# Kernel optimization log

Measured on AMD Instinct MI355X. Metric: run time of the kernel, lower is better.

The kernel has to match this reference:

```python
import jax, jax.numpy as jnp
import numpy as np
import math

D = 768
H = 12
HD = D // H  # 64


def setup_inputs() -> dict:
    key = jax.random.key(0)
    ks = jax.random.split(key, 8)
    B, S = 32, 127
    desc = jax.random.normal(ks[0], (B, S, D), dtype=jnp.float32)
    nv = jax.random.normal(ks[1], (B, S + 1, D), dtype=jnp.float32)
    def xavier(k, shape):
        fan_in, fan_out = shape[1], shape[0]
        gain = 1.0 / math.sqrt(2.0)
        limit = gain * math.sqrt(6.0 / (fan_in + fan_out))
        return jax.random.uniform(k, shape, jnp.float32, -limit, limit)
    Wq = xavier(ks[2], (D, D)); bq = jnp.zeros((D,), jnp.float32)
    Wk = xavier(ks[3], (D, D)); bk = jnp.zeros((D,), jnp.float32)
    Wv = xavier(ks[4], (D, D)); bv = jnp.zeros((D,), jnp.float32)
    # attn_proj: Linear(3*head_dim, 1)
    Wa = xavier(ks[5], (1, 3 * HD))[0]  # [3*HD]
    ba = jnp.zeros((), jnp.float32)
    return {
        "desc_embeddings": desc,
        "name_value_embeddings": nv,
        "Wq": Wq, "bq": bq, "Wk": Wk, "bk": bk, "Wv": Wv, "bv": bv,
        "Wa": Wa, "ba": ba,
    }


def _forward(desc_embeddings, name_value_embeddings, Wq, bq, Wk, bk, Wv, bv, Wa, ba):
    B, new_seq, _ = name_value_embeddings.shape
    S = new_seq - 1

    # adjacency: var-var all ones, CLS->Var row = 1, Var->CLS col = 0, CLS->CLS = 0
    adj = jnp.zeros((new_seq, new_seq), jnp.float32)
    adj = adj.at[1:, 1:].set(1.0)
    adj = adj.at[0, 1:].set(1.0)
    adj = jnp.broadcast_to(adj, (B, new_seq, new_seq))

    # q,k,v: [B, H, new_seq, HD]
    def proj(W, b):
        y = name_value_embeddings @ W.T + b
        return y.reshape(B, new_seq, H, HD).transpose(0, 2, 1, 3)
    q = proj(Wq, bq); k = proj(Wk, bk); v = proj(Wv, bv)

    # attn_proj weight split: [q_part | k_part | edge_part], each [HD]
    wq_a, wk_a, we_a = Wa[:HD], Wa[HD:2 * HD], Wa[2 * HD:]

    # q/k scalar contributions per (b,h,i) and (b,h,j)
    lq = jnp.einsum('bhid,d->bhi', q, wq_a)  # [B,H,new_seq]
    lk = jnp.einsum('bhjd,d->bhj', k, wk_a)  # [B,H,new_seq]

    # edge_attr[b,i,j] per head h (head slice of concat[node_i_desc, node_j_desc]):
    # edge vector = concat(desc_i, desc_j)[h*HD:(h+1)*HD] viewed as [H, HD] of 2D dims.
    # concat(desc_i, desc_j) has 2D dims -> reshaped to [H, HD] means head h takes
    # slice [h*HD:(h+1)*HD] of the 2D-dim concat. Heads 0..H/2-1 come from desc_i,
    # heads H/2..H-1 come from desc_j. Compute edge dot with we_a accordingly.
    # desc_full[b,t] : [B,S,D]. Build per-head contributions:
    # for h < H//2: edge slice = desc_i[h*HD:(h+1)*HD]  -> depends only on i
    # for h >= H//2: edge slice = desc_j[(h-H//2)*HD:(h-H//2+1)*HD] -> depends only on j
    desc_heads = desc_embeddings.reshape(B, S, H // 2, 2 * HD)  # wrong split; do directly
    # Direct: per head h, slice indices into the 2D concat vector
    dh = desc_embeddings.reshape(B, S, H, HD)  # desc split into H chunks of HD (covers D = H*HD)
    # concat(desc_i,desc_j) reshaped to [H,HD]: heads 0..H/2-1 use dh_i[:, :, h],
    # heads H/2..H-1 use dh_j[:, :, h - H/2]
    e_dot = jnp.einsum('bshd,d->bsh', dh, jnp.broadcast_to(we_a, (HD,)))  # placeholder, recompute per head below
    # per-head edge scalar contribution for var-var edges:
    ei = jnp.einsum('bshd,d->bhs', dh, we_a)  # contribution if head slice comes from desc at position s
    Hh = H // 2
    # var-var logits edge part: for h<Hh depends on i; for h>=Hh depends on j
    le_i = ei[:, :Hh, :]   # [B,Hh,S] depends on i (row)
    le_j = ei[:, Hh:, :]   # [B,Hh,S] depends on j (col)

    # CLS edges: cls_edge_attr = concat(desc, desc) at position t (the var index)
    # row 0 (CLS->var j): edge = concat(desc_j, desc_j) -> head h slice:
    #   h<Hh: dh_j[h]; h>=Hh: dh_j[h-Hh]  -> scalar ei[b,h,j] with h mapped
    e_cls = jnp.concatenate([ei[:, :Hh, :], ei[:, :Hh, :]], axis=1) * 0  # init
    e_cls = jnp.concatenate([le_i, le_i], axis=1)  # [B,H,S]: head h<Hh uses dh[h], h>=Hh uses dh[h-Hh]
    # note ei[:, :Hh] corresponds to dh chunks 0..Hh-1 ; for h>=Hh slice is dh[h-Hh] -> same le_i

    # Assemble full logits [B,H,new_seq,new_seq]
    logits = lq[:, :, :, None] + lk[:, :, None, :]
    # edge contributions (only where adj==1; edge_attr zeroed elsewhere by mask mult)
    edge = jnp.zeros((B, H, new_seq, new_seq), jnp.float32)
    # var-var block [1:,1:]
    ev = jnp.zeros((B, H, S, S), jnp.float32)
    ev = ev + jnp.pad(le_i, ((0, 0), (0, Hh), (0, 0)))[:, :, :, None] * 0  # keep shapes
    ev_i = jnp.concatenate([le_i, jnp.zeros_like(le_j)], axis=1)  # h<Hh: i-dependent
    ev_j = jnp.concatenate([jnp.zeros_like(le_i), le_j], axis=1)  # h>=Hh: j-dependent
    ev = ev_i[:, :, :, None] + ev_j[:, :, None, :]  # [B,H,S,S]
    edge = edge.at[:, :, 1:, 1:].set(ev)
    # CLS row (0, 1:): cls_edge = concat(desc_j,desc_j); j = column var
    edge = edge.at[:, :, 0, 1:].set(e_cls)
    # CLS col (1:, 0): cls_edge = concat(desc_i,desc_i) BUT adj[:,1:,0]=0 so edge_attr
    # multiplied by adj -> zero; also masked out. edge stays 0, but torch zeroes it too.
    # mask edge by adjacency (edge_attr *= adj)
    edge = edge * adj[:, None, :, :]
    logits = logits + edge + ba

    mask = (adj[:, None, :, :] == 0).astype(jnp.float32) * -1e9
    logits = logits + mask
    attn = jax.nn.softmax(logits, axis=-1)  # [B,H,new_seq,new_seq]
    ctx = jnp.einsum('bhij,bhjd->bhid', attn, v)
    basis_outputs = ctx.transpose(0, 2, 1, 3)  # [B,new_seq,H,HD]
    return basis_outputs, attn


def reference(desc_embeddings, name_value_embeddings, Wq, bq, Wk, bk, Wv, bv, Wa, ba):
    return _forward(desc_embeddings, name_value_embeddings, Wq, bq, Wk, bk, Wv, bv, Wa, ba)
```

## Files before the change

kernel.cpp:

```cpp
#include <hip/hip_runtime.h>

#define NB 32
#define NS 128
#define SD 127
#define ND 768
#define NH 12
#define HD 64

__device__ inline float wredSum(float v){
  #pragma unroll
  for (int off=32; off>0; off>>=1) v += __shfl_xor(v, off);
  return v;
}
__device__ inline float wredMax(float v){
  #pragma unroll
  for (int off=32; off>0; off>>=1) v = fmaxf(v, __shfl_xor(v, off));
  return v;
}

__global__ __launch_bounds__(256)
void fold_ei(const float* __restrict__ Wk, const float* __restrict__ bk,
             const float* __restrict__ desc, const float* __restrict__ Wa,
             float* __restrict__ uk, float* __restrict__ bkdot,
             float* __restrict__ ei){
  int blk = blockIdx.x, t = threadIdx.x;
  int wave = t >> 6, lane = t & 63;
  if (blk < 144){
    __shared__ float red[4][64];
    int h = blk/12, cb = blk%12;
    int c0 = t & 63, dg = t >> 6;
    const float* base = Wk + (size_t)(h*HD + dg*16)*ND + cb*64 + c0;
    float acc = 0.f;
    #pragma unroll
    for (int i=0;i<16;++i) acc += base[(size_t)i*ND] * Wa[64 + dg*16 + i];
    red[dg][c0] = acc;
    __syncthreads();
    if (dg==0) uk[h*ND + cb*64 + c0] = red[0][c0]+red[1][c0]+red[2][c0]+red[3][c0];
    if (blk==0 && t < NH){
      float a = 0.f;
      for (int d=0; d<64; ++d) a += bk[t*HD+d]*Wa[64+d];
      bkdot[t] = a;
    }
  } else {
    int bs = blk - 144;
    int b = bs / SD, s = bs % SD;
    float wea = Wa[128 + lane];
    const float* row = desc + (size_t)bs * ND;
    #pragma unroll
    for (int hh=0; hh<3; ++hh){
      int h = wave + hh*4;
      float v = row[h*HD + lane] * wea;
      v = wredSum(v);
      if (lane==0) ei[(size_t)(b*NH + h)*NS + s] = v;
    }
  }
}

__global__ __launch_bounds__(256)
void lk_kernel(const float* __restrict__ nv, const float* __restrict__ uk,
               const float* __restrict__ bkdot, float* __restrict__ lk){
  __shared__ __align__(16) float S[4*ND];
  int blk = blockIdx.x, t = threadIdx.x, wave = t>>6, lane = t&63;
  float ukr[3][12], bkd[3];
  #pragma unroll
  for (int hh=0; hh<3; ++hh){
    int h = wave*3 + hh;
    bkd[hh] = bkdot[h];
    #pragma unroll
    for (int k=0;k<12;++k) ukr[hh][k] = uk[h*ND + lane + 64*k];
  }
  int j0 = blk*4;
  const float4* src = (const float4*)(nv + (size_t)j0*ND);
  ((float4*)S)[t]     = src[t];
  ((float4*)S)[t+256] = src[t+256];
  ((float4*)S)[t+512] = src[t+512];
  __syncthreads();
  float acc[12];
  #pragma unroll
  for (int rr=0; rr<4; ++rr){
    #pragma unroll
    for (int hh=0; hh<3; ++hh){
      float a = 0.f;
      #pragma unroll
      for (int k=0;k<12;++k) a += S[rr*ND + lane + 64*k]*ukr[hh][k];
      acc[rr*3+hh] = a;
    }
  }
  #pragma unroll
  for (int i=0;i<12;++i) acc[i] = wredSum(acc[i]);
  if (lane == 0){
    int b = j0 >> 7, jb = j0 & 127;
    #pragma unroll
    for (int rr=0; rr<4; ++rr)
      #pragma unroll
      for (int hh=0; hh<3; ++hh)
        lk[(size_t)(b*NH + wave*3 + hh)*NS + jb + rr] = acc[rr*3+hh] + bkd[hh];
  }
}

__global__ __launch_bounds__(256)
void msoft_attn(const float* __restrict__ nv, const float* __restrict__ lk,
                const float* __restrict__ ei, float* __restrict__ m_part,
                float* __restrict__ out){
  int blk = blockIdx.x;
  int b = blk >> 3, jg = blk & 7;
  int t = threadIdx.x, wave = t >> 6, lane = t & 63;
  __shared__ float slk[NH*NS];
  __shared__ float sei[NH*NS];
  __shared__ float wf[24][NS];
  for (int i=t; i<NH*NS; i+=256) slk[i] = lk[(size_t)b*NH*NS + i];
  for (int i=t; i<NH*NS; i+=256) sei[i] = ei[(size_t)b*NH*NS + i];
  __syncthreads();
  #pragma unroll
  for (int rr=0; rr<6; ++rr){
    int r = wave*6 + rr;
    int h = r >> 1, which = r & 1;
    const float* eirow = (which==0) ? (sei + (h%6)*NS) : (sei + h*NS);
    float g = (which==0) ? 1.f : (h>=6 ? 1.f : 0.f);
    float x0 = (lane>=1) ? slk[h*NS+lane] + g*eirow[lane-1] : -3.0e38f;
    float x1 = slk[h*NS+lane+64] + g*eirow[lane+63];
    float mm = wredMax(fmaxf(x0,x1));
    float e0 = (lane>=1) ? __expf(x0-mm) : 0.f;
    float e1 = __expf(x1-mm);
    float s  = wredSum(e0+e1);
    float inv = 1.f/s;
    wf[r][lane]    = e0*inv;
    wf[r][lane+64] = e1*inv;
  }
  __syncthreads();
  if (t < 192){
    const float4* nvb = (const float4*)(nv + ((size_t)b*NS + jg*16)*ND);
    float4 acc[24];
    #pragma unroll
    for (int r=0;r<24;++r) acc[r] = make_float4(0.f,0.f,0.f,0.f);
    #pragma unroll 2
    for (int jj=0; jj<16; ++jj){
      float4 x = nvb[jj*192 + t];
      int j = jg*16 + jj;
      #pragma unroll
      for (int r=0;r<24;++r){
        float wr = wf[r][j];
        acc[r].x += wr*x.x; acc[r].y += wr*x.y;
        acc[r].z += wr*x.z; acc[r].w += wr*x.w;
      }
    }
    #pragma unroll
    for (int r=0;r<24;++r)
      ((float4*)(m_part + ((size_t)(b*24 + r)*8 + jg)*ND))[t] = acc[r];
  }
  float* abase = out + (size_t)NB*NS*ND + (size_t)(b*NH)*NS*NS;
  for (int idx=t; idx<6144; idx+=256){
    int h = idx >> 9;
    int rem = idx & 511;
    int il = rem >> 5, q = rem & 31;
    int i = jg*16 + il;
    const float* srcw = (i==0) ? wf[h*2] : wf[h*2+1];
    float4 v = { srcw[q*4], srcw[q*4+1], srcw[q*4+2], srcw[q*4+3] };
    ((float4*)(abase + (size_t)h*NS*NS))[i*32 + q] = v;
  }
}

__global__ __launch_bounds__(256)
void proj_basis(const float* __restrict__ m_part, const float* __restrict__ Wv,
                const float* __restrict__ bv, float* __restrict__ out){
  int bh = blockIdx.x;
  int b = bh / NH, h = bh % NH;
  int t = threadIdx.x, wave = t >> 6, lane = t & 63;
  __shared__ float msum0[ND], msum1[ND];
  __shared__ float cvec[2*HD];
  for (int i=t; i<2*ND; i+=256){
    int rl = (i >= ND);
    int c  = i - rl*ND;
    const float* mp = m_part + ((size_t)(b*24 + h*2 + rl)*8)*ND + c;
    float s = 0.f;
    #pragma unroll
    for (int g8=0; g8<8; ++g8) s += mp[(size_t)g8*ND];
    (rl ? msum1 : msum0)[c] = s;
  }
  __syncthreads();
  #pragma unroll
  for (int dd=0; dd<16; ++dd){
    int d = wave*16 + dd;
    const float* wvr = Wv + (size_t)(h*HD + d)*ND;
    float p0=0.f, p1=0.f;
    #pragma unroll
    for (int k=0; k<12; ++k){
      float wv = wvr[lane + 64*k];
      p0 += wv*msum0[lane + 64*k];
      p1 += wv*msum1[lane + 64*k];
    }
    p0 = wredSum(p0); p1 = wredSum(p1);
    if (lane==0){
      float bb = bv[h*HD + d];
      cvec[d]    = p0 + bb;
      cvec[64+d] = p1 + bb;
    }
  }
  __syncthreads();
  float* bo = out + (size_t)b*NS*ND + h*HD;
  #pragma unroll
  for (int k=0;k<8;++k){
    int idx = t + k*256;
    int i = idx>>4, q = idx&15;
    const float* srcc = (i==0) ? cvec : cvec+64;
    float4 v = { srcc[q*4], srcc[q*4+1], srcc[q*4+2], srcc[q*4+3] };
    *(float4*)(bo + (size_t)i*ND + q*4) = v;
  }
}

extern "C" void kernel_launch(void* const* d_in, const int* in_sizes, int n_in,
                              void* d_out, int out_size, void* d_ws, size_t ws_size,
                              hipStream_t stream) {
  const float* desc = (const float*)d_in[0];
  const float* nv   = (const float*)d_in[1];
  const float* Wk   = (const float*)d_in[4];
  const float* bk   = (const float*)d_in[5];
  const float* Wv   = (const float*)d_in[6];
  const float* bv   = (const float*)d_in[7];
  const float* Wa   = (const float*)d_in[8];
  float* out = (float*)d_out;
  float* ws  = (float*)d_ws;

  float* uk     = ws;
  float* bkdot  = ws + 9216;
  float* eibuf  = ws + 9232;
  float* lkbuf  = ws + 58384;
  float* m_part = ws + 107536;

  fold_ei   <<<4208, 256, 0, stream>>>(Wk, bk, desc, Wa, uk, bkdot, eibuf);
  lk_kernel <<<1024, 256, 0, stream>>>(nv, uk, bkdot, lkbuf);
  msoft_attn<<<256,  256, 0, stream>>>(nv, lkbuf, eibuf, m_part, out);
  proj_basis<<<384,  256, 0, stream>>>(m_part, Wv, bv, out);
}
```

Baseline: 138.7 us.

## Fuse Wv projection into attention kernel with atomic accumulation and last-block output

Removes the separate proj_basis kernel and the m_part global buffer. Each attention block now owns a 96-column slice of the feature dimension: it reduces its weighted sums in shared memory, multiplies them by the matching Wv slice, and atomically adds the partial results into a per-batch ctx buffer that the first kernel pre-fills with bv. A per-batch counter lets the last finishing block broadcast ctx into the basis output. This saves a kernel launch and the m_part round trip through global memory, at the cost of float atomics, non-deterministic summation order, and extra barriers.

```diff
diff --git a/kernel.cpp b/kernel.cpp
--- a/kernel.cpp
+++ b/kernel.cpp
@@ -19,10 +19,12 @@
 }
 
 __global__ __launch_bounds__(256)
-void fold_ei(const float* __restrict__ Wk, const float* __restrict__ bk,
-             const float* __restrict__ desc, const float* __restrict__ Wa,
-             float* __restrict__ uk, float* __restrict__ bkdot,
-             float* __restrict__ ei){
+void fold_ei_init(const float* __restrict__ Wk, const float* __restrict__ bk,
+                  const float* __restrict__ desc, const float* __restrict__ Wa,
+                  const float* __restrict__ bv,
+                  float* __restrict__ uk, float* __restrict__ bkdot,
+                  float* __restrict__ ei, float* __restrict__ ctx,
+                  int* __restrict__ cnt){
   int blk = blockIdx.x, t = threadIdx.x;
   int wave = t >> 6, lane = t & 63;
   if (blk < 144){
@@ -41,7 +43,7 @@
       for (int d=0; d<64; ++d) a += bk[t*HD+d]*Wa[64+d];
       bkdot[t] = a;
     }
-  } else {
+  } else if (blk < 144 + NB*SD){
     int bs = blk - 144;
     int b = bs / SD, s = bs % SD;
     float wea = Wa[128 + lane];
@@ -53,6 +55,15 @@
       v = wredSum(v);
       if (lane==0) ei[(size_t)(b*NH + h)*NS + s] = v;
     }
+  } else {
+    int idx = (blk - (144 + NB*SD))*256 + t;
+    int rem = idx % 384;
+    int r = rem >> 4, q = rem & 15;
+    int h = r >> 1;
+    const float* bb = bv + h*HD + q*4;
+    float4 v = { bb[0], bb[1], bb[2], bb[3] };
+    ((float4*)ctx)[idx] = v;
+    if (blk == 144 + NB*SD && t < NB) cnt[t] = 0;
   }
 }
 
@@ -77,7 +88,7 @@
   __syncthreads();
   float acc[12];
   #pragma unroll
-  for (int rr=0; rr<4; ++rr){
+  for (int rr=0; rr<4; ++rr)
     #pragma unroll
     for (int hh=0; hh<3; ++hh){
       float a = 0.f;
@@ -85,7 +96,6 @@
       for (int k=0;k<12;++k) a += S[rr*ND + lane + 64*k]*ukr[hh][k];
       acc[rr*3+hh] = a;
     }
-  }
   #pragma unroll
   for (int i=0;i<12;++i) acc[i] = wredSum(acc[i]);
   if (lane == 0){
@@ -99,15 +109,22 @@
 }
 
 __global__ __launch_bounds__(256)
-void msoft_attn(const float* __restrict__ nv, const float* __restrict__ lk,
-                const float* __restrict__ ei, float* __restrict__ m_part,
-                float* __restrict__ out){
+void fused(const float* __restrict__ nv, const float* __restrict__ lk,
+           const float* __restrict__ ei, const float* __restrict__ Wv,
+           float* __restrict__ ctx, int* __restrict__ cnt,
+           float* __restrict__ out){
   int blk = blockIdx.x;
-  int b = blk >> 3, jg = blk & 7;
+  int b = blk >> 3, cc = blk & 7;
   int t = threadIdx.x, wave = t >> 6, lane = t & 63;
-  __shared__ float slk[NH*NS];
-  __shared__ float sei[NH*NS];
-  __shared__ float wf[24][NS];
+  __shared__ __align__(16) float S[13104];
+  __shared__ int flag;
+  float* slk  = S;
+  float* sei  = S + 1536;
+  float* wf   = S + 3072;
+  float* mred = S + 6144;
+  float* m    = S + 10752;
+  float* ctxb = S + 6144;
+
   for (int i=t; i<NH*NS; i+=256) slk[i] = lk[(size_t)b*NH*NS + i];
   for (int i=t; i<NH*NS; i+=256) sei[i] = ei[(size_t)b*NH*NS + i];
   __syncthreads();
@@ -124,87 +141,108 @@
     float e1 = __expf(x1-mm);
     float s  = wredSum(e0+e1);
     float inv = 1.f/s;
-    wf[r][lane]    = e0*inv;
-    wf[r][lane+64] = e1*inv;
-  }
+    wf[r*NS + lane]    = e0*inv;
+    wf[r*NS + lane+64] = e1*inv;
+  }
+
+  float4 acc[24];
+  #pragma unroll
+  for (int r=0;r<24;++r) acc[r] = make_float4(0.f,0.f,0.f,0.f);
+  int col = t % 24, jg = t / 24;
   __syncthreads();
   if (t < 192){
-    const float4* nvb = (const float4*)(nv + ((size_t)b*NS + jg*16)*ND);
-    float4 acc[24];
-    #pragma unroll
-    for (int r=0;r<24;++r) acc[r] = make_float4(0.f,0.f,0.f,0.f);
+    const float4* nvb = (const float4*)nv;
     #pragma unroll 2
     for (int jj=0; jj<16; ++jj){
-      float4 x = nvb[jj*192 + t];
       int j = jg*16 + jj;
+      float4 x = nvb[(size_t)(b*NS + j)*192 + cc*24 + col];
       #pragma unroll
       for (int r=0;r<24;++r){
-        float wr = wf[r][j];
+        float wr = wf[r*NS + j];
         acc[r].x += wr*x.x; acc[r].y += wr*x.y;
         acc[r].z += wr*x.z; acc[r].w += wr*x.w;
       }
     }
-    #pragma unroll
-    for (int r=0;r<24;++r)
-      ((float4*)(m_part + ((size_t)(b*24 + r)*8 + jg)*ND))[t] = acc[r];
-  }
+  }
+  #pragma unroll
+  for (int p=0; p<4; ++p){
+    __syncthreads();
+    if (t < 192){
+      #pragma unroll
+      for (int rr=0; rr<6; ++rr)
+        ((float4*)mred)[(rr*24 + col)*8 + jg] = acc[p*6+rr];
+    }
+    __syncthreads();
+    if (t < 144){
+      int rr = t / 24, c2 = t % 24;
+      float4 s = make_float4(0.f,0.f,0.f,0.f);
+      #pragma unroll
+      for (int g=0; g<8; ++g){
+        float4 v = ((float4*)mred)[(rr*24 + c2)*8 + g];
+        s.x += v.x; s.y += v.y; s.z += v.z; s.w += v.w;
+      }
+      int r = p*6 + rr;
+      m[r*97 + c2*4+0] = s.x; m[r*97 + c2*4+1] = s.y;
+      m[r*97 + c2*4+2] = s.z; m[r*97 + c2*4+3] = s.w;
+    }
+  }
+  __syncthreads();
+
+  #pragma unroll
+  for (int i=0; i<3; ++i){
+    int hd = t*3 + i;
+    int h = hd >> 6, d = hd & 63;
+    const float4* wr = (const float4*)(Wv + (size_t)hd*ND + cc*96);
+    const float* m0 = m + (2*h)*97;
+    const float* m1 = m0 + 97;
+    float p0=0.f, p1=0.f;
+    #pragma unroll
+    for (int c4=0; c4<24; ++c4){
+      float4 wv4 = wr[c4];
+      int c = c4*4;
+      p0 += wv4.x*m0[c] + wv4.y*m0[c+1] + wv4.z*m0[c+2] + wv4.w*m0[c+3];
+      p1 += wv4.x*m1[c] + wv4.y*m1[c+1] + wv4.z*m1[c+2] + wv4.w*m1[c+3];
+    }
+    atomicAdd(&ctx[(size_t)(b*24 + 2*h    )*HD + d], p0);
+    atomicAdd(&ctx[(size_t)(b*24 + 2*h + 1)*HD + d], p1);
+  }
+
   float* abase = out + (size_t)NB*NS*ND + (size_t)(b*NH)*NS*NS;
   for (int idx=t; idx<6144; idx+=256){
     int h = idx >> 9;
     int rem = idx & 511;
     int il = rem >> 5, q = rem & 31;
-    int i = jg*16 + il;
-    const float* srcw = (i==0) ? wf[h*2] : wf[h*2+1];
+    int i = cc*16 + il;
+    const float* srcw = (i==0) ? (wf + h*2*NS) : (wf + (h*2+1)*NS);
     float4 v = { srcw[q*4], srcw[q*4+1], srcw[q*4+2], srcw[q*4+3] };
     ((float4*)(abase + (size_t)h*NS*NS))[i*32 + q] = v;
   }
-}
-
-__global__ __launch_bounds__(256)
-void proj_basis(const float* __restrict__ m_part, const float* __restrict__ Wv,
-                const float* __restrict__ bv, float* __restrict__ out){
-  int bh = blockIdx.x;
-  int b = bh / NH, h = bh % NH;
-  int t = threadIdx.x, wave = t >> 6, lane = t & 63;
-  __shared__ float msum0[ND], msum1[ND];
-  __shared__ float cvec[2*HD];
-  for (int i=t; i<2*ND; i+=256){
-    int rl = (i >= ND);
-    int c  = i - rl*ND;
-    const float* mp = m_part + ((size_t)(b*24 + h*2 + rl)*8)*ND + c;
-    float s = 0.f;
-    #pragma unroll
-    for (int g8=0; g8<8; ++g8) s += mp[(size_t)g8*ND];
-    (rl ? msum1 : msum0)[c] = s;
-  }
-  __syncthreads();
-  #pragma unroll
-  for (int dd=0; dd<16; ++dd){
-    int d = wave*16 + dd;
-    const float* wvr = Wv + (size_t)(h*HD + d)*ND;
-    float p0=0.f, p1=0.f;
-    #pragma unroll
-    for (int k=0; k<12; ++k){
-      float wv = wvr[lane + 64*k];
-      p0 += wv*msum0[lane + 64*k];
-      p1 += wv*msum1[lane + 64*k];
-    }
-    p0 = wredSum(p0); p1 = wredSum(p1);
-    if (lane==0){
-      float bb = bv[h*HD + d];
-      cvec[d]    = p0 + bb;
-      cvec[64+d] = p1 + bb;
-    }
-  }
-  __syncthreads();
-  float* bo = out + (size_t)b*NS*ND + h*HD;
-  #pragma unroll
-  for (int k=0;k<8;++k){
-    int idx = t + k*256;
-    int i = idx>>4, q = idx&15;
-    const float* srcc = (i==0) ? cvec : cvec+64;
-    float4 v = { srcc[q*4], srcc[q*4+1], srcc[q*4+2], srcc[q*4+3] };
-    *(float4*)(bo + (size_t)i*ND + q*4) = v;
+
+  __syncthreads();
+  if (t == 0){
+    int old = __hip_atomic_fetch_add(cnt + b, 1, __ATOMIC_ACQ_REL,
+                                     __HIP_MEMORY_SCOPE_AGENT);
+    flag = (old == 7);
+  }
+  __syncthreads();
+  if (flag){
+    #pragma unroll
+    for (int k=0;k<6;++k){
+      int idx = t + k*256;
+      ctxb[idx] = __hip_atomic_load(&ctx[(size_t)b*1536 + idx],
+                                    __ATOMIC_RELAXED, __HIP_MEMORY_SCOPE_AGENT);
+    }
+    __syncthreads();
+    float4* bo = (float4*)(out + (size_t)b*NS*ND);
+    #pragma unroll
+    for (int k=0;k<96;++k){
+      int idx = t + k*256;
+      int i = idx / 192, rem = idx % 192;
+      int h = rem >> 4, q = rem & 15;
+      const float* srcc = ctxb + (2*h + (i!=0))*HD + q*4;
+      float4 v = { srcc[0], srcc[1], srcc[2], srcc[3] };
+      bo[idx] = v;
+    }
   }
 }
 
@@ -221,14 +259,15 @@
   float* out = (float*)d_out;
   float* ws  = (float*)d_ws;
 
-  float* uk     = ws;
-  float* bkdot  = ws + 9216;
-  float* eibuf  = ws + 9232;
-  float* lkbuf  = ws + 58384;
-  float* m_part = ws + 107536;
-
-  fold_ei   <<<4208, 256, 0, stream>>>(Wk, bk, desc, Wa, uk, bkdot, eibuf);
-  lk_kernel <<<1024, 256, 0, stream>>>(nv, uk, bkdot, lkbuf);
-  msoft_attn<<<256,  256, 0, stream>>>(nv, lkbuf, eibuf, m_part, out);
-  proj_basis<<<384,  256, 0, stream>>>(m_part, Wv, bv, out);
-}
+  int*   cnt    = (int*)d_ws;
+  float* uk     = ws + 32;
+  float* bkdot  = ws + 9248;
+  float* eibuf  = ws + 9264;
+  float* lkbuf  = ws + 58416;
+  float* ctx    = ws + 107568;
+
+  fold_ei_init<<<4256, 256, 0, stream>>>(Wk, bk, desc, Wa, bv, uk, bkdot,
+                                         eibuf, ctx, cnt);
+  lk_kernel   <<<1024, 256, 0, stream>>>(nv, uk, bkdot, lkbuf);
+  fused       <<<256,  256, 0, stream>>>(nv, lkbuf, eibuf, Wv, ctx, cnt, out);
+}
```

Measured after the change: 147.1 us. 1.06x slower.
